# Kernel optimization log

Measured on AMD Instinct MI355X. Metric: run time of the kernel, lower is better.

## Reference

```python
import jax, jax.numpy as jnp
import numpy as np

FRAME, PROJ, MID, HID, T, B = 2048, 512, 128, 1024, 48, 512


def _uniform(key, shape, stdv):
    return jax.random.uniform(key, shape, jnp.float32, -stdv, stdv)


def setup_inputs() -> dict:
    key = jax.random.key(0)
    ks = jax.random.split(key, 16)
    sp = 1.0 / np.sqrt(FRAME)   # frame_embed init
    s1 = 1.0 / np.sqrt(HID)     # LSTMCell init (1/sqrt(hidden))
    sbd = 1.0 / np.sqrt(PROJ)   # BoundaryDetector init (1/sqrt(i_features))
    return {
        "video_feats": jax.random.normal(ks[0], (B, T, FRAME), jnp.float32),
        # frame_embed: Linear(frame_size, projected_size)
        "We": _uniform(ks[1], (PROJ, FRAME), sp),
        "be": _uniform(ks[2], (PROJ,), sp),
        # lstm1: LSTMCell(projected, hidden) with bias
        "W1_ih": _uniform(ks[3], (4 * HID, PROJ), s1),
        "W1_hh": _uniform(ks[4], (4 * HID, HID), s1),
        "b1_ih": _uniform(ks[5], (4 * HID,), s1),
        "b1_hh": _uniform(ks[6], (4 * HID,), s1),
        # lstm2: LSTMCell(hidden, hidden), bias=False
        "W2_ih": _uniform(ks[7], (4 * HID, HID), s1),
        "W2_hh": _uniform(ks[8], (4 * HID, HID), s1),
        # BoundaryDetector params
        "Wsi": _uniform(ks[9], (MID, PROJ), sbd),
        "Wsh": _uniform(ks[10], (MID, HID), sbd),
        "bbd": _uniform(ks[11], (MID,), sbd),
        "vs": _uniform(ks[12], (1, MID), sbd),
    }


def _lstm_cell(x, h, c, W_ih, W_hh, b):
    gates = x @ W_ih.T + h @ W_hh.T + b  # [B, 4H]
    i, f, g, o = jnp.split(gates, 4, axis=-1)  # PyTorch gate order i,f,g,o
    i, f, o = jax.nn.sigmoid(i), jax.nn.sigmoid(f), jax.nn.sigmoid(o)
    g = jnp.tanh(g)
    c_new = f * c + i * g
    h_new = o * jnp.tanh(c_new)
    return h_new, c_new


def _binary_gate(z):
    # eval mode: threshold 0.5; straight-through identity backward
    hard = (z > 0.5).astype(z.dtype)
    return z + jax.lax.stop_gradient(hard - z)


def reference(video_feats, We, be, W1_ih, W1_hh, b1_ih, b1_hh, W2_ih, W2_hh, Wsi, Wsh, bbd, vs):
    bsz = video_feats.shape[0]
    # frame embedding (dropout is identity in eval mode)
    v = video_feats @ We.T + be  # [B, T, PROJ]
    v_t = jnp.swapaxes(v, 0, 1)  # [T, B, PROJ]
    b1 = b1_ih + b1_hh
    zeros = jnp.zeros((bsz, HID), video_feats.dtype)

    def step(carry, vt):
        h1, c1, h2, c2 = carry
        z = jax.nn.sigmoid((vt @ Wsi.T + h1 @ Wsh.T + bbd) @ vs.T)  # [B, 1]
        s = _binary_gate(z)
        h1n, c1n = _lstm_cell(vt, h1, c1, W1_ih, W1_hh, b1)
        h2n, c2n = _lstm_cell(h1n * s, h2, c2, W2_ih, W2_hh, 0.0)
        h1n = h1n * (1.0 - s)
        c1n = c1n * (1.0 - s)
        return (h1n, c1n, h2n, c2n), None

    (h1, _, _, _), _ = jax.lax.scan(step, (zeros, zeros, zeros, zeros), v_t)
    return h1
```

## Files before the change

### kernel.cpp

```cpp
#include <hip/hip_runtime.h>

#define B_     512
#define T_     48
#define FRAME_ 2048
#define PROJ_  512
#define MID_   128
#define HID_   1024
#define G4_    4096

typedef unsigned short u16;
typedef __bf16 bf16x8 __attribute__((ext_vector_type(8)));
typedef float  f32x4  __attribute__((ext_vector_type(4)));

__device__ __forceinline__ float sigmoidf_(float x) {
    return 1.0f / (1.0f + expf(-x));
}
__device__ __forceinline__ u16 f2bf_rn(float f) {
    unsigned int u = __float_as_uint(f);
    u += 0x7fffu + ((u >> 16) & 1u);
    return (u16)(u >> 16);
}
__device__ __forceinline__ float bf2f(u16 s) {
    return __uint_as_float(((unsigned int)s) << 16);
}
__device__ __forceinline__ void gld16(const void* g, void* l) {
    __builtin_amdgcn_global_load_lds((const __attribute__((address_space(1))) void*)g,
                                     (__attribute__((address_space(3))) void*)l, 16, 0, 0);
}
__device__ __forceinline__ uint4 pack8(const u16* h) {
    return make_uint4((unsigned)h[0] | ((unsigned)h[1] << 16),
                      (unsigned)h[2] | ((unsigned)h[3] << 16),
                      (unsigned)h[4] | ((unsigned)h[5] << 16),
                      (unsigned)h[6] | ((unsigned)h[7] << 16));
}

__global__ void wvec_kernel(const float* __restrict__ Wsi, const float* __restrict__ Wsh,
                            const float* __restrict__ vs,
                            double* __restrict__ wsi_vd, float* __restrict__ wsh_v)
{
    const int gid = blockIdx.x * 256 + threadIdx.x;
    if (gid < 512) {
        double s = 0.0;
        for (int mi = 0; mi < MID_; ++mi)
            s += (double)vs[mi] * (double)Wsi[(size_t)mi * PROJ_ + gid];
        wsi_vd[gid] = s;
    } else if (gid < 1536) {
        const int k = gid - 512;
        double s = 0.0;
        for (int mi = 0; mi < MID_; ++mi)
            s += (double)vs[mi] * (double)Wsh[(size_t)mi * HID_ + k];
        wsh_v[k] = (float)s;
    }
}

__global__ void cc_kernel(const float* __restrict__ be, const double* __restrict__ wsi_vd,
                          const float* __restrict__ vs, const float* __restrict__ bbd,
                          double* __restrict__ cc)
{
    __shared__ double red[256];
    const int tid = threadIdx.x;
    double s = 0.0;
    for (int p = tid; p < PROJ_; p += 256) s += (double)be[p] * wsi_vd[p];
    red[tid] = s;
    __syncthreads();
    for (int st = 128; st > 0; st >>= 1) {
        if (tid < st) red[tid] += red[tid + st];
        __syncthreads();
    }
    if (tid == 0) {
        double b = 0.0;
        for (int mi = 0; mi < MID_; ++mi) b += (double)vs[mi] * (double)bbd[mi];
        cc[0] = red[0] + b;
    }
}

__global__ void u_kernel(const float* __restrict__ We, const double* __restrict__ wsi_vd,
                         double* __restrict__ u)
{
    const int f = blockIdx.x * 256 + threadIdx.x;
    double s = 0.0;
    for (int p = 0; p < PROJ_; ++p)
        s += wsi_vd[p] * (double)We[(size_t)p * FRAME_ + f];
    u[f] = s;
}

__global__ __launch_bounds__(256)
void vidpack_kernel(const float* __restrict__ video, const double* __restrict__ u,
                    const double* __restrict__ cc,
                    u16* __restrict__ phi, u16* __restrict__ plo,
                    float* __restrict__ Lv)
{
    __shared__ double red[16][17];
    const int tid = threadIdx.x;
    const int r   = tid & 15, kq = tid >> 4;
    const int row = blockIdx.x * 16 + r;
    const float* vr = video + (size_t)row * FRAME_;
    double s = 0.0;
#pragma unroll
    for (int j = 0; j < 16; ++j) {
        const int k0 = kq * 128 + j * 8;
        const float4 a = *(const float4*)&vr[k0];
        const float4 b = *(const float4*)&vr[k0 + 4];
        const float f[8] = {a.x, a.y, a.z, a.w, b.x, b.y, b.z, b.w};
        s += (double)f[0]*u[k0+0] + (double)f[1]*u[k0+1] + (double)f[2]*u[k0+2]
           + (double)f[3]*u[k0+3] + (double)f[4]*u[k0+4] + (double)f[5]*u[k0+5]
           + (double)f[6]*u[k0+6] + (double)f[7]*u[k0+7];
        u16 h[8], l[8];
#pragma unroll
        for (int e = 0; e < 8; ++e) {
            h[e] = f2bf_rn(f[e]);
            l[e] = f2bf_rn(f[e] - bf2f(h[e]));
        }
        const int g = kq * 16 + j;
        const size_t off = ((size_t)g * 24576 + row) * 16;
        *(uint4*)((char*)phi + off) = pack8(h);
        *(uint4*)((char*)plo + off) = pack8(l);
    }
    red[r][kq] = s;
    __syncthreads();
    if (tid < 16) {
        double t = 0.0;
#pragma unroll
        for (int q = 0; q < 16; ++q) t += red[tid][q];
        const int rw = blockIdx.x * 16 + tid;
        Lv[(rw % T_) * B_ + rw / T_] = (float)(t + cc[0]);
    }
}

__global__ void wepack_kernel(const float* __restrict__ We,
                              u16* __restrict__ phi, u16* __restrict__ plo)
{
    const int kk = blockIdx.x, by = blockIdx.y, tid = threadIdx.x;
#pragma unroll
    for (int pass = 0; pass < 2; ++pass) {
        const int g = tid + pass * 256;
        const int ko = g >> 7, n = g & 127;
        const int p = by * 128 + n;
        const int k = kk * 32 + ko * 8;
        const float4 a = *(const float4*)&We[(size_t)p * FRAME_ + k];
        const float4 b = *(const float4*)&We[(size_t)p * FRAME_ + k + 4];
        const float f[8] = {a.x, a.y, a.z, a.w, b.x, b.y, b.z, b.w};
        u16 h[8], l[8];
#pragma unroll
        for (int e = 0; e < 8; ++e) {
            h[e] = f2bf_rn(f[e]);
            l[e] = f2bf_rn(f[e] - bf2f(h[e]));
        }
        const size_t off = (((size_t)by * 64 + kk) * 512 + g) * 16;
        *(uint4*)((char*)phi + off) = pack8(h);
        *(uint4*)((char*)plo + off) = pack8(l);
    }
}

__global__ void wihpack_kernel(const float* __restrict__ Wih,
                               u16* __restrict__ phi, u16* __restrict__ plo)
{
    const int kk = blockIdx.x, by = blockIdx.y, tid = threadIdx.x;
#pragma unroll
    for (int pass = 0; pass < 2; ++pass) {
        const int g = tid + pass * 256;
        const int ko = g >> 7, n = g & 127;
        const int gate = n & 3, hl = n >> 2;
        const int srow = gate * HID_ + by * 32 + hl;
        const int k = kk * 32 + ko * 8;
        const float4 a = *(const float4*)&Wih[(size_t)srow * PROJ_ + k];
        const float4 b = *(const float4*)&Wih[(size_t)srow * PROJ_ + k + 4];
        const float f[8] = {a.x, a.y, a.z, a.w, b.x, b.y, b.z, b.w};
        u16 h[8], l[8];
#pragma unroll
        for (int e = 0; e < 8; ++e) {
            h[e] = f2bf_rn(f[e]);
            l[e] = f2bf_rn(f[e] - bf2f(h[e]));
        }
        const size_t off = (((size_t)by * 16 + kk) * 512 + g) * 16;
        *(uint4*)((char*)phi + off) = pack8(h);
        *(uint4*)((char*)plo + off) = pack8(l);
    }
}

__global__ void whhpack_kernel(const float* __restrict__ Whh,
                               u16* __restrict__ phi, u16* __restrict__ plo)
{
    const int kk = blockIdx.x, by = blockIdx.y, tid = threadIdx.x;
#pragma unroll
    for (int pass = 0; pass < 2; ++pass) {
        const int g = tid + pass * 256;
        const int ko = g >> 7, n = g & 127;
        const int gate = n & 3, hl = n >> 2;
        const int srow = gate * HID_ + by * 32 + hl;
        const int k = kk * 32 + ko * 8;
        const float4 a = *(const float4*)&Whh[(size_t)srow * HID_ + k];
        const float4 b = *(const float4*)&Whh[(size_t)srow * HID_ + k + 4];
        const float f[8] = {a.x, a.y, a.z, a.w, b.x, b.y, b.z, b.w};
        u16 h[8], l[8];
#pragma unroll
        for (int e = 0; e < 8; ++e) {
            h[e] = f2bf_rn(f[e]);
            l[e] = f2bf_rn(f[e] - bf2f(h[e]));
        }
        const size_t off = (((size_t)by * 32 + kk) * 512 + g) * 16;
        *(uint4*)((char*)phi + off) = pack8(h);
        *(uint4*)((char*)plo + off) = pack8(l);
    }
}

__global__ void b1g_kernel(const float* __restrict__ bih, const float* __restrict__ bhh,
                           float* __restrict__ b1g)
{
    const int n = blockIdx.x * 256 + threadIdx.x;
    const int by = n >> 7, nl = n & 127;
    const int gate = nl & 3, hl = nl >> 2;
    const int src = gate * HID_ + by * 32 + hl;
    b1g[n] = bih[src] + bhh[src];
}


__global__ __launch_bounds__(256, 2)
void embed_mfma_kernel(const u16* __restrict__ Ahi_g, const u16* __restrict__ Alo_g,
                       const u16* __restrict__ Bhi_g, const u16* __restrict__ Blo_g,
                       const float* __restrict__ be,
                       u16* __restrict__ vphi, u16* __restrict__ vplo)
{
    __shared__ char smem[65536];
    const int tid = threadIdx.x;
    const int xcd = blockIdx.x & 7, s_ = blockIdx.x >> 3;
    const int by = s_ & 3, bx = xcd * 24 + (s_ >> 2);
    const int n0 = by * 128, row0 = bx * 128;
    const int w = tid >> 6, l = tid & 63, lm = l & 15, ko4 = l >> 4;
    const int wr = (w >> 1) * 64, wc = (w & 1) * 64;

    const char* aS[4]; const char* bS[4]; int loff[4];
#pragma unroll
    for (int i = 0; i < 4; ++i) {
        const int j = w * 4 + i;
        const int ip = (j & 7) * 64 + l;
        const int ko = ip >> 7, rc = ip & 127;
        const char* ab = (j >> 3) ? (const char*)Alo_g : (const char*)Ahi_g;
        aS[i] = ab + ((size_t)ko * 24576 + row0 + rc) * 16;
        const char* bb = (j >> 3) ? (const char*)Blo_g : (const char*)Bhi_g;
        bS[i] = bb + (size_t)by * 524288 + (size_t)ip * 16;
        loff[i] = j * 1024 + l * 16;
    }

    f32x4 acc[4][4] = {};
#pragma unroll
    for (int i = 0; i < 4; ++i) {
        gld16(aS[i], smem + loff[i]);
        gld16(bS[i], smem + 16384 + loff[i]);
    }

#pragma unroll 2
    for (int kk = 0; kk < 64; ++kk) {
        if (kk + 1 < 64) {
            const int bo = ((kk + 1) & 1) * 32768;
#pragma unroll
            for (int i = 0; i < 4; ++i) {
                gld16(aS[i] + (size_t)(kk + 1) * 1572864, smem + bo + loff[i]);
                gld16(bS[i] + (size_t)(kk + 1) * 8192,    smem + bo + 16384 + loff[i]);
            }
            asm volatile("s_waitcnt vmcnt(8)\ns_barrier" ::: "memory");
        } else {
            asm volatile("s_waitcnt vmcnt(0)\ns_barrier" ::: "memory");
        }
        __builtin_amdgcn_sched_barrier(0);

        const char* rb = smem + (kk & 1) * 32768;
        bf16x8 Ah[4], Al[4], Bh[4], Bl[4];
#pragma unroll
        for (int mt = 0; mt < 4; ++mt) {
            const int idx = (ko4 * 128 + wr + mt * 16 + lm) * 16;
            Ah[mt] = *(const bf16x8*)(rb + idx);
            Al[mt] = *(const bf16x8*)(rb + 8192 + idx);
        }
#pragma unroll
        for (int nt = 0; nt < 4; ++nt) {
            const int idx = (ko4 * 128 + wc + nt * 16 + lm) * 16;
            Bh[nt] = *(const bf16x8*)(rb + 16384 + idx);
            Bl[nt] = *(const bf16x8*)(rb + 24576 + idx);
        }
        asm volatile("s_waitcnt lgkmcnt(0)\ns_barrier" ::: "memory");
        __builtin_amdgcn_sched_barrier(0);
#pragma unroll
        for (int mt = 0; mt < 4; ++mt)
#pragma unroll
            for (int nt = 0; nt < 4; ++nt) {
                acc[mt][nt] = __builtin_amdgcn_mfma_f32_16x16x32_bf16(Ah[mt], Bh[nt], acc[mt][nt], 0, 0, 0);
                acc[mt][nt] = __builtin_amdgcn_mfma_f32_16x16x32_bf16(Ah[mt], Bl[nt], acc[mt][nt], 0, 0, 0);
                acc[mt][nt] = __builtin_amdgcn_mfma_f32_16x16x32_bf16(Al[mt], Bh[nt], acc[mt][nt], 0, 0, 0);
            }
    }

    __syncthreads();
    float* S = (float*)smem;
#pragma unroll
    for (int h = 0; h < 2; ++h) {
        if ((w >> 1) == h) {
#pragma unroll
            for (int mt = 0; mt < 4; ++mt)
#pragma unroll
                for (int nt = 0; nt < 4; ++nt)
#pragma unroll
                    for (int r = 0; r < 4; ++r)
                        S[(mt * 16 + ko4 * 4 + r) * 132 + wc + nt * 16 + lm] = acc[mt][nt][r];
        }
        __syncthreads();
#pragma unroll
        for (int i = 0; i < 4; ++i) {
            const int task = tid * 4 + i;
            const int m = task >> 4, gr = task & 15;
            const int p0 = n0 + gr * 8;
            const float4 s0 = *(const float4*)&S[m * 132 + gr * 8];
            const float4 s1 = *(const float4*)&S[m * 132 + gr * 8 + 4];
            const float4 e0 = *(const float4*)&be[p0];
            const float4 e1 = *(const float4*)&be[p0 + 4];
            const float o[8] = {s0.x + e0.x, s0.y + e0.y, s0.z + e0.z, s0.w + e0.w,
                                s1.x + e1.x, s1.y + e1.y, s1.z + e1.z, s1.w + e1.w};
            u16 hb[8], lb[8];
#pragma unroll
            for (int e = 0; e < 8; ++e) {
                hb[e] = f2bf_rn(o[e]);
                lb[e] = f2bf_rn(o[e] - bf2f(hb[e]));
            }
            const int R = row0 + h * 64 + m;
            const int t = R % T_, b = R / T_;
            const size_t off = (size_t)t * 524288 + (((size_t)(p0 >> 3)) * 512 + b) * 16;
            *(uint4*)((char*)vphi + off) = pack8(hb);
            *(uint4*)((char*)vplo + off) = pack8(lb);
        }
        __syncthreads();
    }
}

__global__ __launch_bounds__(256, 2)
void gx_mfma_kernel(const u16* __restrict__ vphi, const u16* __restrict__ vplo,
                    const u16* __restrict__ Wihhi, const u16* __restrict__ Wihlo,
                    const float* __restrict__ b1g, float* __restrict__ Gx)
{
    __shared__ char smem[65536];
    const int tid = threadIdx.x;
    const int xcd = blockIdx.x & 7, s_ = blockIdx.x >> 3;
    const int by = s_ & 31;
    const int tile = xcd * 24 + (s_ >> 5);
    const int t2 = tile >> 2, b0 = (tile & 3) * 128;
    const int n0 = by * 128;
    const int w = tid >> 6, l = tid & 63, lm = l & 15, ko4 = l >> 4;
    const int wr = (w >> 1) * 64, wc = (w & 1) * 64;

    const char* aS[4]; const char* bS[4]; int loff[4];
#pragma unroll
    for (int i = 0; i < 4; ++i) {
        const int j = w * 4 + i;
        const int ip = (j & 7) * 64 + l;
        const int ko = ip >> 7, rc = ip & 127;
        const char* ab = ((j >> 3) ? (const char*)vplo : (const char*)vphi)
                         + (size_t)t2 * 524288;
        aS[i] = ab + ((size_t)ko * 512 + b0 + rc) * 16;
        const char* bb = (j >> 3) ? (const char*)Wihlo : (const char*)Wihhi;
        bS[i] = bb + (size_t)by * 131072 + (size_t)ip * 16;
        loff[i] = j * 1024 + l * 16;
    }

    f32x4 acc[4][4] = {};
#pragma unroll
    for (int i = 0; i < 4; ++i) {
        gld16(aS[i], smem + loff[i]);
        gld16(bS[i], smem + 16384 + loff[i]);
    }

#pragma unroll 2
    for (int kk = 0; kk < 16; ++kk) {
        if (kk + 1 < 16) {
            const int bo = ((kk + 1) & 1) * 32768;
#pragma unroll
            for (int i = 0; i < 4; ++i) {
                gld16(aS[i] + (size_t)(kk + 1) * 32768, smem + bo + loff[i]);
                gld16(bS[i] + (size_t)(kk + 1) * 8192,  smem + bo + 16384 + loff[i]);
            }
            asm volatile("s_waitcnt vmcnt(8)\ns_barrier" ::: "memory");
        } else {
            asm volatile("s_waitcnt vmcnt(0)\ns_barrier" ::: "memory");
        }
        __builtin_amdgcn_sched_barrier(0);

        const char* rb = smem + (kk & 1) * 32768;
        bf16x8 Ah[4], Al[4], Bh[4], Bl[4];
#pragma unroll
        for (int mt = 0; mt < 4; ++mt) {
            const int idx = (ko4 * 128 + wr + mt * 16 + lm) * 16;
            Ah[mt] = *(const bf16x8*)(rb + idx);
            Al[mt] = *(const bf16x8*)(rb + 8192 + idx);
        }
#pragma unroll
        for (int nt = 0; nt < 4; ++nt) {
            const int idx = (ko4 * 128 + wc + nt * 16 + lm) * 16;
            Bh[nt] = *(const bf16x8*)(rb + 16384 + idx);
            Bl[nt] = *(const bf16x8*)(rb + 24576 + idx);
        }
        asm volatile("s_waitcnt lgkmcnt(0)\ns_barrier" ::: "memory");
        __builtin_amdgcn_sched_barrier(0);
#pragma unroll
        for (int mt = 0; mt < 4; ++mt)
#pragma unroll
            for (int nt = 0; nt < 4; ++nt) {
                acc[mt][nt] = __builtin_amdgcn_mfma_f32_16x16x32_bf16(Ah[mt], Bh[nt], acc[mt][nt], 0, 0, 0);
                acc[mt][nt] = __builtin_amdgcn_mfma_f32_16x16x32_bf16(Ah[mt], Bl[nt], acc[mt][nt], 0, 0, 0);
                acc[mt][nt] = __builtin_amdgcn_mfma_f32_16x16x32_bf16(Al[mt], Bh[nt], acc[mt][nt], 0, 0, 0);
            }
    }

    float bg[4];
#pragma unroll
    for (int nt = 0; nt < 4; ++nt) bg[nt] = b1g[n0 + wc + nt * 16 + lm];
    float* gbase = Gx + ((size_t)t2 * 512 + b0) * 4096 + n0;
#pragma unroll
    for (int mt = 0; mt < 4; ++mt)
#pragma unroll
        for (int r = 0; r < 4; ++r) {
            const int row = wr + mt * 16 + ko4 * 4 + r;
            float* rp = gbase + (size_t)row * 4096 + wc;
#pragma unroll
            for (int nt = 0; nt < 4; ++nt)
                __builtin_nontemporal_store(acc[mt][nt][r] + bg[nt], rp + nt * 16 + lm);
        }
}

__global__ __launch_bounds__(512, 2)
void lstm_mfma_kernel(const u16* __restrict__ hhi,  const u16* __restrict__ hlo,
                      const u16* __restrict__ Whhhi, const u16* __restrict__ Whhlo,
                      const float* __restrict__ Gxt,
                      const float* __restrict__ Lv_t,
                      const float* __restrict__ Pin,
                      float* __restrict__ Pout,
                      const float* __restrict__ wsh_v,
                      float* __restrict__ c1, float* __restrict__ h1o,
                      u16* __restrict__ hhio, u16* __restrict__ hloo)
{
    __shared__ char smem[65792];
    float* keepsm = (float*)(smem + 65536);
    const int tid = threadIdx.x;
    const int bid = blockIdx.x;
    const int xcd = bid & 7, slot = bid >> 3;
    const int by  = xcd * 4 + (slot & 3);
    const int bx  = slot >> 2;
    const int b0  = bx * 64;
    const int w = tid >> 6, l = tid & 63, lm = l & 15, ko4 = l >> 4;
    const int wr = (w >> 2) * 32, wc = (w & 3) * 32;
    const int t8 = tid & 255;
    const int koA = t8 >> 6, am = t8 & 63;

    if (tid < 64) {
        double s = (double)Lv_t[b0 + tid];
#pragma unroll
        for (int j = 0; j < 32; ++j) s += (double)Pin[j * B_ + b0 + tid];
        keepsm[tid] = (s > 0.0) ? 0.0f : 1.0f;
    }

    const char* aH = (const char*)(tid < 256 ? hhi : hlo)
                     + ((size_t)koA * 512 + b0 + am) * 16;
    const char* bh = (const char*)Whhhi + (size_t)by * 262144
                     + ((size_t)(ko4 * 128 + wc + lm)) * 16;
    const char* bl = (const char*)Whhlo + (size_t)by * 262144
                     + ((size_t)(ko4 * 128 + wc + lm)) * 16;
    char* lbase = smem + (tid >> 8) * 4096 + t8 * 16;

    f32x4 acc[2][2] = {};
    bf16x8 nBh[2][2], nBl[2][2], cBh[2][2], cBl[2][2], fAh[2][2], fAl[2][2];

    gld16(aH + (size_t)0 * 32768, lbase);
    gld16(aH + (size_t)1 * 32768, lbase + 8192);
    gld16(aH + (size_t)2 * 32768, lbase + 16384);
    gld16(aH + (size_t)3 * 32768, lbase + 16384 + 8192);
#pragma unroll
    for (int h = 0; h < 2; ++h)
#pragma unroll
        for (int nt = 0; nt < 2; ++nt) {
            nBh[h][nt] = *(const bf16x8*)(bh + (size_t)h * 8192 + nt * 256);
            nBl[h][nt] = *(const bf16x8*)(bl + (size_t)h * 8192 + nt * 256);
        }

#pragma unroll
    for (int kk = 0; kk < 16; ++kk) {
        if (kk == 15) asm volatile("s_waitcnt vmcnt(8)\ns_barrier" ::: "memory");
        else          asm volatile("s_waitcnt vmcnt(10)\ns_barrier" ::: "memory");
        __builtin_amdgcn_sched_barrier(0);
#pragma unroll
        for (int h = 0; h < 2; ++h)
#pragma unroll
            for (int nt = 0; nt < 2; ++nt) {
                cBh[h][nt] = nBh[h][nt]; cBl[h][nt] = nBl[h][nt];
            }
        const char* rb = smem + (kk & 3) * 16384;
#pragma unroll
        for (int h = 0; h < 2; ++h)
#pragma unroll
            for (int mt = 0; mt < 2; ++mt) {
                const int idx = (ko4 * 64 + wr + mt * 16 + lm) * 16;
                fAh[h][mt] = *(const bf16x8*)(rb + h * 8192 + idx);
                fAl[h][mt] = *(const bf16x8*)(rb + h * 8192 + 4096 + idx);
            }
        if (kk + 1 < 16) {
#pragma unroll
            for (int h = 0; h < 2; ++h)
#pragma unroll
                for (int nt = 0; nt < 2; ++nt) {
                    nBh[h][nt] = *(const bf16x8*)(bh + (size_t)(2 * (kk + 1) + h) * 8192 + nt * 256);
                    nBl[h][nt] = *(const bf16x8*)(bl + (size_t)(2 * (kk + 1) + h) * 8192 + nt * 256);
                }
        }
        if (kk + 2 < 16) {
            char* db = smem + ((kk + 2) & 3) * 16384 + (tid >> 8) * 4096 + t8 * 16;
            gld16(aH + (size_t)(2 * (kk + 2) + 0) * 32768, db);
            gld16(aH + (size_t)(2 * (kk + 2) + 1) * 32768, db + 8192);
        }
#pragma unroll
        for (int h = 0; h < 2; ++h)
#pragma unroll
            for (int mt = 0; mt < 2; ++mt)
#pragma unroll
                for (int nt = 0; nt < 2; ++nt) {
                    acc[mt][nt] = __builtin_amdgcn_mfma_f32_16x16x32_bf16(fAh[h][mt], cBh[h][nt], acc[mt][nt], 0, 0, 0);
                    acc[mt][nt] = __builtin_amdgcn_mfma_f32_16x16x32_bf16(fAh[h][mt], cBl[h][nt], acc[mt][nt], 0, 0, 0);
                    acc[mt][nt] = __builtin_amdgcn_mfma_f32_16x16x32_bf16(fAl[h][mt], cBh[h][nt], acc[mt][nt], 0, 0, 0);
                }
    }
    asm volatile("s_waitcnt lgkmcnt(0)" ::: "memory");
    __builtin_amdgcn_sched_barrier(0);

    const int h_l = tid & 31, rg = tid >> 5;
    const int hg  = by * 32 + h_l;
    float4 gx[4];
#pragma unroll
    for (int i = 0; i < 4; ++i)
        gx[i] = *(const float4*)&Gxt[((size_t)b0 + rg * 4 + i) * 4096 + by * 128 + h_l * 4];

    __syncthreads();
    float* S = (float*)smem;
#pragma unroll
    for (int mt = 0; mt < 2; ++mt)
#pragma unroll
        for (int nt = 0; nt < 2; ++nt) {
            const int col = wc + nt * 16 + lm;
#pragma unroll
            for (int r = 0; r < 4; ++r) {
                const int row = wr + mt * 16 + ko4 * 4 + r;
                S[row * 132 + col] = acc[mt][nt][r];
            }
        }
    __syncthreads();

    const float wv = wsh_v[hg];
    const size_t hgbase = (((size_t)by * 4 + (h_l >> 3)) * 512) * 16 + (h_l & 7) * 2;
#pragma unroll
    for (int i = 0; i < 4; ++i) {
        const int m = rg * 4 + i;
        const int b = b0 + m;
        const float4 g4 = *(const float4*)&S[m * 132 + h_l * 4];
        const float i_ = sigmoidf_(g4.x + gx[i].x);
        const float f_ = sigmoidf_(g4.y + gx[i].y);
        const float g_ = tanhf(g4.z + gx[i].z);
        const float o_ = sigmoidf_(g4.w + gx[i].w);
        const size_t off = (size_t)b * HID_ + hg;
        float cn = f_ * c1[off] + i_ * g_;
        float hn = o_ * tanhf(cn);
        const float kp = keepsm[m];
        cn *= kp; hn *= kp;
        c1[off] = cn;
        if (h1o) h1o[off] = hn;
        const u16 hb = f2bf_rn(hn);
        const size_t hoff = hgbase + (size_t)b * 16;
        *(u16*)((char*)hhio + hoff) = hb;
        *(u16*)((char*)hloo + hoff) = f2bf_rn(hn - bf2f(hb));
        float pr = hn * wv;
        pr += __shfl_xor(pr, 16);
        pr += __shfl_xor(pr, 8);
        pr += __shfl_xor(pr, 4);
        pr += __shfl_xor(pr, 2);
        pr += __shfl_xor(pr, 1);
        if (h_l == 0) Pout[by * B_ + b] = pr;
    }
}

extern "C" void kernel_launch(void* const* d_in, const int* in_sizes, int n_in,
                              void* d_out, int out_size, void* d_ws, size_t ws_size,
                              hipStream_t stream)
{
    const float* video = (const float*)d_in[0];
    const float* We    = (const float*)d_in[1];
    const float* be    = (const float*)d_in[2];
    const float* W1_ih = (const float*)d_in[3];
    const float* W1_hh = (const float*)d_in[4];
    const float* b1_ih = (const float*)d_in[5];
    const float* b1_hh = (const float*)d_in[6];
    const float* Wsi   = (const float*)d_in[9];
    const float* Wsh   = (const float*)d_in[10];
    const float* bbd   = (const float*)d_in[11];
    const float* vs    = (const float*)d_in[12];
    float* out = (float*)d_out;

    char* p = (char*)d_ws;
    auto alloc = [&](size_t bytes) { char* r = p; p += (bytes + 255) & ~(size_t)255; return r; };
    u16* vidhi = (u16*)alloc((size_t)24576 * FRAME_ * 2);
    u16* vidlo = (u16*)alloc((size_t)24576 * FRAME_ * 2);
    u16* vphi  = (u16*)alloc((size_t)T_ * B_ * PROJ_ * 2);
    u16* vplo  = (u16*)alloc((size_t)T_ * B_ * PROJ_ * 2);
    u16* Wehi  = (u16*)alloc((size_t)PROJ_ * FRAME_ * 2);
    u16* Welo  = (u16*)alloc((size_t)PROJ_ * FRAME_ * 2);
    u16* Wihhi = (u16*)alloc((size_t)G4_ * PROJ_ * 2);
    u16* Wihlo = (u16*)alloc((size_t)G4_ * PROJ_ * 2);
    u16* Whhhi = (u16*)alloc((size_t)G4_ * HID_ * 2);
    u16* Whhlo = (u16*)alloc((size_t)G4_ * HID_ * 2);
    float* Gx  = (float*)alloc((size_t)T_ * B_ * G4_ * 4);
    float* c1  = (float*)alloc((size_t)B_ * HID_ * 4);
    u16* hhiA  = (u16*)alloc((size_t)B_ * HID_ * 2);
    u16* hhiB  = (u16*)alloc((size_t)B_ * HID_ * 2);
    u16* hloA  = (u16*)alloc((size_t)B_ * HID_ * 2);
    u16* hloB  = (u16*)alloc((size_t)B_ * HID_ * 2);
    double* wsi_vd = (double*)alloc(512 * 8);
    double* ud     = (double*)alloc(2048 * 8);
    double* ccd    = (double*)alloc(256);
    float* wsh_v = (float*)alloc(1024 * 4);
    float* Lv    = (float*)alloc((size_t)T_ * B_ * 4);
    float* PA    = (float*)alloc(32 * B_ * 4);
    float* PB    = (float*)alloc(32 * B_ * 4);
    float* b1g   = (float*)alloc(G4_ * 4);

    (void)hipMemsetAsync(c1,   0, (size_t)B_ * HID_ * 4, stream);
    (void)hipMemsetAsync(hhiA, 0, (size_t)B_ * HID_ * 2, stream);
    (void)hipMemsetAsync(hloA, 0, (size_t)B_ * HID_ * 2, stream);
    (void)hipMemsetAsync(PA,   0, 32 * B_ * 4, stream);

    b1g_kernel<<<16, 256, 0, stream>>>(b1_ih, b1_hh, b1g);
    wvec_kernel<<<6, 256, 0, stream>>>(Wsi, Wsh, vs, wsi_vd, wsh_v);
    cc_kernel<<<1, 256, 0, stream>>>(be, wsi_vd, vs, bbd, ccd);
    u_kernel<<<8, 256, 0, stream>>>(We, wsi_vd, ud);
    wepack_kernel<<<dim3(64, 4), 256, 0, stream>>>(We, Wehi, Welo);
    wihpack_kernel<<<dim3(16, 32), 256, 0, stream>>>(W1_ih, Wihhi, Wihlo);
    whhpack_kernel<<<dim3(32, 32), 256, 0, stream>>>(W1_hh, Whhhi, Whhlo);
    vidpack_kernel<<<1536, 256, 0, stream>>>(video, ud, ccd, vidhi, vidlo, Lv);
    embed_mfma_kernel<<<768, 256, 0, stream>>>(vidhi, vidlo, Wehi, Welo, be, vphi, vplo);
    gx_mfma_kernel<<<6144, 256, 0, stream>>>(vphi, vplo, Wihhi, Wihlo, b1g, Gx);

    u16* hhi_in = hhiA; u16* hhi_out = hhiB;
    u16* hlo_in = hloA; u16* hlo_out = hloB;
    float* Pin = PA; float* Pout = PB;

    for (int t = 0; t < T_; ++t) {
        float* ho = (t == T_ - 1) ? out : nullptr;
        lstm_mfma_kernel<<<256, 512, 0, stream>>>(hhi_in, hlo_in, Whhhi, Whhlo,
                                                  Gx + (size_t)t * B_ * G4_,
                                                  Lv + t * B_, Pin, Pout, wsh_v,
                                                  c1, ho, hhi_out, hlo_out);
        { u16* tmp = hhi_in; hhi_in = hhi_out; hhi_out = tmp; }
        { u16* tmp = hlo_in; hlo_in = hlo_out; hlo_out = tmp; }
        { float* tmp = Pin; Pin = Pout; Pout = tmp; }
    }
}
```

Measured before the change: 1.636 ms.

## Fuse input-gate GEMM into per-step LSTM kernel, drop Gx precompute

Removes the separate gx_mfma kernel that precomputed x@W_ih for all timesteps into a large fp32 Gx buffer (T*B*4096 floats). Each per-timestep LSTM kernel now extends its K loop from 16 to 24 iterations, streaming the bf16 hi/lo projected input and W_ih alongside h and W_hh, and adds only the bias. This avoids writing and rereading roughly 400MB of Gx, at the cost of adding the input GEMM to the serial recurrent critical path, where it may be less efficient than the batched version.

```diff
diff --git a/kernel.cpp b/kernel.cpp
--- a/kernel.cpp
+++ b/kernel.cpp
@@ -214,7 +214,6 @@
     b1g[n] = bih[src] + bhh[src];
 }
 
-
 __global__ __launch_bounds__(256, 2)
 void embed_mfma_kernel(const u16* __restrict__ Ahi_g, const u16* __restrict__ Alo_g,
                        const u16* __restrict__ Bhi_g, const u16* __restrict__ Blo_g,
@@ -331,103 +330,12 @@
     }
 }
 
-__global__ __launch_bounds__(256, 2)
-void gx_mfma_kernel(const u16* __restrict__ vphi, const u16* __restrict__ vplo,
-                    const u16* __restrict__ Wihhi, const u16* __restrict__ Wihlo,
-                    const float* __restrict__ b1g, float* __restrict__ Gx)
-{
-    __shared__ char smem[65536];
-    const int tid = threadIdx.x;
-    const int xcd = blockIdx.x & 7, s_ = blockIdx.x >> 3;
-    const int by = s_ & 31;
-    const int tile = xcd * 24 + (s_ >> 5);
-    const int t2 = tile >> 2, b0 = (tile & 3) * 128;
-    const int n0 = by * 128;
-    const int w = tid >> 6, l = tid & 63, lm = l & 15, ko4 = l >> 4;
-    const int wr = (w >> 1) * 64, wc = (w & 1) * 64;
-
-    const char* aS[4]; const char* bS[4]; int loff[4];
-#pragma unroll
-    for (int i = 0; i < 4; ++i) {
-        const int j = w * 4 + i;
-        const int ip = (j & 7) * 64 + l;
-        const int ko = ip >> 7, rc = ip & 127;
-        const char* ab = ((j >> 3) ? (const char*)vplo : (const char*)vphi)
-                         + (size_t)t2 * 524288;
-        aS[i] = ab + ((size_t)ko * 512 + b0 + rc) * 16;
-        const char* bb = (j >> 3) ? (const char*)Wihlo : (const char*)Wihhi;
-        bS[i] = bb + (size_t)by * 131072 + (size_t)ip * 16;
-        loff[i] = j * 1024 + l * 16;
-    }
-
-    f32x4 acc[4][4] = {};
-#pragma unroll
-    for (int i = 0; i < 4; ++i) {
-        gld16(aS[i], smem + loff[i]);
-        gld16(bS[i], smem + 16384 + loff[i]);
-    }
-
-#pragma unroll 2
-    for (int kk = 0; kk < 16; ++kk) {
-        if (kk + 1 < 16) {
-            const int bo = ((kk + 1) & 1) * 32768;
-#pragma unroll
-            for (int i = 0; i < 4; ++i) {
-                gld16(aS[i] + (size_t)(kk + 1) * 32768, smem + bo + loff[i]);
-                gld16(bS[i] + (size_t)(kk + 1) * 8192,  smem + bo + 16384 + loff[i]);
-            }
-            asm volatile("s_waitcnt vmcnt(8)\ns_barrier" ::: "memory");
-        } else {
-            asm volatile("s_waitcnt vmcnt(0)\ns_barrier" ::: "memory");
-        }
-        __builtin_amdgcn_sched_barrier(0);
-
-        const char* rb = smem + (kk & 1) * 32768;
-        bf16x8 Ah[4], Al[4], Bh[4], Bl[4];
-#pragma unroll
-        for (int mt = 0; mt < 4; ++mt) {
-            const int idx = (ko4 * 128 + wr + mt * 16 + lm) * 16;
-            Ah[mt] = *(const bf16x8*)(rb + idx);
-            Al[mt] = *(const bf16x8*)(rb + 8192 + idx);
-        }
-#pragma unroll
-        for (int nt = 0; nt < 4; ++nt) {
-            const int idx = (ko4 * 128 + wc + nt * 16 + lm) * 16;
-            Bh[nt] = *(const bf16x8*)(rb + 16384 + idx);
-            Bl[nt] = *(const bf16x8*)(rb + 24576 + idx);
-        }
-        asm volatile("s_waitcnt lgkmcnt(0)\ns_barrier" ::: "memory");
-        __builtin_amdgcn_sched_barrier(0);
-#pragma unroll
-        for (int mt = 0; mt < 4; ++mt)
-#pragma unroll
-            for (int nt = 0; nt < 4; ++nt) {
-                acc[mt][nt] = __builtin_amdgcn_mfma_f32_16x16x32_bf16(Ah[mt], Bh[nt], acc[mt][nt], 0, 0, 0);
-                acc[mt][nt] = __builtin_amdgcn_mfma_f32_16x16x32_bf16(Ah[mt], Bl[nt], acc[mt][nt], 0, 0, 0);
-                acc[mt][nt] = __builtin_amdgcn_mfma_f32_16x16x32_bf16(Al[mt], Bh[nt], acc[mt][nt], 0, 0, 0);
-            }
-    }
-
-    float bg[4];
-#pragma unroll
-    for (int nt = 0; nt < 4; ++nt) bg[nt] = b1g[n0 + wc + nt * 16 + lm];
-    float* gbase = Gx + ((size_t)t2 * 512 + b0) * 4096 + n0;
-#pragma unroll
-    for (int mt = 0; mt < 4; ++mt)
-#pragma unroll
-        for (int r = 0; r < 4; ++r) {
-            const int row = wr + mt * 16 + ko4 * 4 + r;
-            float* rp = gbase + (size_t)row * 4096 + wc;
-#pragma unroll
-            for (int nt = 0; nt < 4; ++nt)
-                __builtin_nontemporal_store(acc[mt][nt][r] + bg[nt], rp + nt * 16 + lm);
-        }
-}
-
 __global__ __launch_bounds__(512, 2)
-void lstm_mfma_kernel(const u16* __restrict__ hhi,  const u16* __restrict__ hlo,
+void lstm_mfma_kernel(const u16* __restrict__ vthi, const u16* __restrict__ vtlo,
+                      const u16* __restrict__ hhi,  const u16* __restrict__ hlo,
+                      const u16* __restrict__ Wihhi, const u16* __restrict__ Wihlo,
                       const u16* __restrict__ Whhhi, const u16* __restrict__ Whhlo,
-                      const float* __restrict__ Gxt,
+                      const float* __restrict__ b1g,
                       const float* __restrict__ Lv_t,
                       const float* __restrict__ Pin,
                       float* __restrict__ Pout,
@@ -455,32 +363,44 @@
         keepsm[tid] = (s > 0.0) ? 0.0f : 1.0f;
     }
 
-    const char* aH = (const char*)(tid < 256 ? hhi : hlo)
-                     + ((size_t)koA * 512 + b0 + am) * 16;
-    const char* bh = (const char*)Whhhi + (size_t)by * 262144
-                     + ((size_t)(ko4 * 128 + wc + lm)) * 16;
-    const char* bl = (const char*)Whhlo + (size_t)by * 262144
-                     + ((size_t)(ko4 * 128 + wc + lm)) * 16;
+    const size_t aoff = ((size_t)koA * 512 + b0 + am) * 16;
+    const char* aV = (const char*)(tid < 256 ? vthi : vtlo) + aoff;
+    const char* aH = (const char*)(tid < 256 ? hhi  : hlo ) + aoff;
+    const size_t boff = ((size_t)(ko4 * 128 + wc + lm)) * 16;
+    const char* bIhH = (const char*)Wihhi + (size_t)by * 131072 + boff;
+    const char* bIhL = (const char*)Wihlo + (size_t)by * 131072 + boff;
+    const char* bHhH = (const char*)Whhhi + (size_t)by * 262144 + boff;
+    const char* bHhL = (const char*)Whhlo + (size_t)by * 262144 + boff;
     char* lbase = smem + (tid >> 8) * 4096 + t8 * 16;
+
+    auto aSrc = [&](int g) {
+        return (g < 16) ? aV + (size_t)g * 32768 : aH + (size_t)(g - 16) * 32768;
+    };
+    auto bSrcH = [&](int g) {
+        return (g < 16) ? bIhH + (size_t)g * 8192 : bHhH + (size_t)(g - 16) * 8192;
+    };
+    auto bSrcL = [&](int g) {
+        return (g < 16) ? bIhL + (size_t)g * 8192 : bHhL + (size_t)(g - 16) * 8192;
+    };
 
     f32x4 acc[2][2] = {};
     bf16x8 nBh[2][2], nBl[2][2], cBh[2][2], cBl[2][2], fAh[2][2], fAl[2][2];
 
-    gld16(aH + (size_t)0 * 32768, lbase);
-    gld16(aH + (size_t)1 * 32768, lbase + 8192);
-    gld16(aH + (size_t)2 * 32768, lbase + 16384);
-    gld16(aH + (size_t)3 * 32768, lbase + 16384 + 8192);
+    gld16(aSrc(0), lbase);
+    gld16(aSrc(1), lbase + 8192);
+    gld16(aSrc(2), lbase + 16384);
+    gld16(aSrc(3), lbase + 16384 + 8192);
 #pragma unroll
     for (int h = 0; h < 2; ++h)
 #pragma unroll
         for (int nt = 0; nt < 2; ++nt) {
-            nBh[h][nt] = *(const bf16x8*)(bh + (size_t)h * 8192 + nt * 256);
-            nBl[h][nt] = *(const bf16x8*)(bl + (size_t)h * 8192 + nt * 256);
-        }
-
-#pragma unroll
-    for (int kk = 0; kk < 16; ++kk) {
-        if (kk == 15) asm volatile("s_waitcnt vmcnt(8)\ns_barrier" ::: "memory");
+            nBh[h][nt] = *(const bf16x8*)(bSrcH(h) + nt * 256);
+            nBl[h][nt] = *(const bf16x8*)(bSrcL(h) + nt * 256);
+        }
+
+#pragma unroll
+    for (int kk = 0; kk < 24; ++kk) {
+        if (kk == 23) asm volatile("s_waitcnt vmcnt(8)\ns_barrier" ::: "memory");
         else          asm volatile("s_waitcnt vmcnt(10)\ns_barrier" ::: "memory");
         __builtin_amdgcn_sched_barrier(0);
 #pragma unroll
@@ -498,19 +418,19 @@
                 fAh[h][mt] = *(const bf16x8*)(rb + h * 8192 + idx);
                 fAl[h][mt] = *(const bf16x8*)(rb + h * 8192 + 4096 + idx);
             }
-        if (kk + 1 < 16) {
+        if (kk + 1 < 24) {
 #pragma unroll
             for (int h = 0; h < 2; ++h)
 #pragma unroll
                 for (int nt = 0; nt < 2; ++nt) {
-                    nBh[h][nt] = *(const bf16x8*)(bh + (size_t)(2 * (kk + 1) + h) * 8192 + nt * 256);
-                    nBl[h][nt] = *(const bf16x8*)(bl + (size_t)(2 * (kk + 1) + h) * 8192 + nt * 256);
+                    nBh[h][nt] = *(const bf16x8*)(bSrcH(2 * (kk + 1) + h) + nt * 256);
+                    nBl[h][nt] = *(const bf16x8*)(bSrcL(2 * (kk + 1) + h) + nt * 256);
                 }
         }
-        if (kk + 2 < 16) {
+        if (kk + 2 < 24) {
             char* db = smem + ((kk + 2) & 3) * 16384 + (tid >> 8) * 4096 + t8 * 16;
-            gld16(aH + (size_t)(2 * (kk + 2) + 0) * 32768, db);
-            gld16(aH + (size_t)(2 * (kk + 2) + 1) * 32768, db + 8192);
+            gld16(aSrc(2 * (kk + 2) + 0), db);
+            gld16(aSrc(2 * (kk + 2) + 1), db + 8192);
         }
 #pragma unroll
         for (int h = 0; h < 2; ++h)
@@ -528,10 +448,7 @@
 
     const int h_l = tid & 31, rg = tid >> 5;
     const int hg  = by * 32 + h_l;
-    float4 gx[4];
-#pragma unroll
-    for (int i = 0; i < 4; ++i)
-        gx[i] = *(const float4*)&Gxt[((size_t)b0 + rg * 4 + i) * 4096 + by * 128 + h_l * 4];
+    const float4 bgv = *(const float4*)&b1g[by * 128 + h_l * 4];
 
     __syncthreads();
     float* S = (float*)smem;
@@ -555,10 +472,10 @@
         const int m = rg * 4 + i;
         const int b = b0 + m;
         const float4 g4 = *(const float4*)&S[m * 132 + h_l * 4];
-        const float i_ = sigmoidf_(g4.x + gx[i].x);
-        const float f_ = sigmoidf_(g4.y + gx[i].y);
-        const float g_ = tanhf(g4.z + gx[i].z);
-        const float o_ = sigmoidf_(g4.w + gx[i].w);
+        const float i_ = sigmoidf_(g4.x + bgv.x);
+        const float f_ = sigmoidf_(g4.y + bgv.y);
+        const float g_ = tanhf(g4.z + bgv.z);
+        const float o_ = sigmoidf_(g4.w + bgv.w);
         const size_t off = (size_t)b * HID_ + hg;
         float cn = f_ * c1[off] + i_ * g_;
         float hn = o_ * tanhf(cn);
@@ -609,7 +526,6 @@
     u16* Wihlo = (u16*)alloc((size_t)G4_ * PROJ_ * 2);
     u16* Whhhi = (u16*)alloc((size_t)G4_ * HID_ * 2);
     u16* Whhlo = (u16*)alloc((size_t)G4_ * HID_ * 2);
-    float* Gx  = (float*)alloc((size_t)T_ * B_ * G4_ * 4);
     float* c1  = (float*)alloc((size_t)B_ * HID_ * 4);
     u16* hhiA  = (u16*)alloc((size_t)B_ * HID_ * 2);
     u16* hhiB  = (u16*)alloc((size_t)B_ * HID_ * 2);
@@ -638,16 +554,17 @@
     whhpack_kernel<<<dim3(32, 32), 256, 0, stream>>>(W1_hh, Whhhi, Whhlo);
     vidpack_kernel<<<1536, 256, 0, stream>>>(video, ud, ccd, vidhi, vidlo, Lv);
     embed_mfma_kernel<<<768, 256, 0, stream>>>(vidhi, vidlo, Wehi, Welo, be, vphi, vplo);
-    gx_mfma_kernel<<<6144, 256, 0, stream>>>(vphi, vplo, Wihhi, Wihlo, b1g, Gx);
 
     u16* hhi_in = hhiA; u16* hhi_out = hhiB;
     u16* hlo_in = hloA; u16* hlo_out = hloB;
     float* Pin = PA; float* Pout = PB;
 
     for (int t = 0; t < T_; ++t) {
+        const u16* vthi = vphi + (size_t)t * 262144;
+        const u16* vtlo = vplo + (size_t)t * 262144;
         float* ho = (t == T_ - 1) ? out : nullptr;
-        lstm_mfma_kernel<<<256, 512, 0, stream>>>(hhi_in, hlo_in, Whhhi, Whhlo,
-                                                  Gx + (size_t)t * B_ * G4_,
+        lstm_mfma_kernel<<<256, 512, 0, stream>>>(vthi, vtlo, hhi_in, hlo_in,
+                                                  Wihhi, Wihlo, Whhhi, Whhlo, b1g,
                                                   Lv + t * B_, Pin, Pout, wsh_v,
                                                   c1, ho, hhi_out, hlo_out);
         { u16* tmp = hhi_in; hhi_in = hhi_out; hhi_out = tmp; }
```

New measurement: 1.587 ms. 3.0% less time.
